# Kernel optimization log

Measured on AMD Instinct MI355X. Metric: run time of the kernel, lower is better.

The kernel has to match this reference:

```python
import jax, jax.numpy as jnp
import numpy as np

B, N, D, HID, S, NH = 2, 384, 768, 256, 64, 8


def layernorm(x, g, b, eps=1e-5):
    m = x.mean(-1, keepdims=True)
    v = ((x - m) ** 2).mean(-1, keepdims=True)
    return (x - m) * jax.lax.rsqrt(v + eps) * g + b


def setup_inputs() -> dict:
    key = jax.random.key(0)
    ks = jax.random.split(key, 32)
    r = lambda i, shp: jax.random.normal(ks[i], shp, dtype=jnp.float32) * 0.02
    inp = {
        'coordinates': jax.random.normal(ks[0], (B, N, 3), dtype=jnp.float32),
        'features': jax.random.normal(ks[1], (B, N, D), dtype=jnp.float32),
        'superpoint_labels': jax.random.randint(ks[2], (B, N), 0, S),
        # geometric_encoder: Linear(9,HID)-LN-ReLU-Linear(HID,D)-LN
        'ge_w1': r(3, (9, HID)), 'ge_b1': jnp.zeros((HID,)),
        'ge_g1': jnp.ones((HID,)), 'ge_be1': jnp.zeros((HID,)),
        'ge_w2': r(4, (HID, D)), 'ge_b2': jnp.zeros((D,)),
        'ge_g2': jnp.ones((D,)), 'ge_be2': jnp.zeros((D,)),
        # superpoint_aggregator: Linear(D,HID)-LN-ReLU-Linear(HID,D)-LN
        'ag_w1': r(5, (D, HID)), 'ag_b1': jnp.zeros((HID,)),
        'ag_g1': jnp.ones((HID,)), 'ag_be1': jnp.zeros((HID,)),
        'ag_w2': r(6, (HID, D)), 'ag_b2': jnp.zeros((D,)),
        'ag_g2': jnp.ones((D,)), 'ag_be2': jnp.zeros((D,)),
        # spatial_attention (MultiheadAttention, 8 heads)
        'wq': r(7, (D, D)), 'bq': jnp.zeros((D,)),
        'wk': r(8, (D, D)), 'bk': jnp.zeros((D,)),
        'wv': r(9, (D, D)), 'bv': jnp.zeros((D,)),
        'wo': r(10, (D, D)), 'bo': jnp.zeros((D,)),
    }
    return inp


def _forward(coordinates, features, superpoint_labels,
             ge_w1, ge_b1, ge_g1, ge_be1, ge_w2, ge_b2, ge_g2, ge_be2,
             ag_w1, ag_b1, ag_g1, ag_be1, ag_w2, ag_b2, ag_g2, ag_be2,
             wq, bq, wk, bk, wv, bv, wo, bo):
    # pairwise geometric relations: [B,N,N,9]
    rp = coordinates[:, :, None, :] - coordinates[:, None, :, :]
    dist = jnp.linalg.norm(rp, axis=-1, keepdims=True)
    rn = rp / jnp.maximum(dist, 1e-12)  # F.normalize semantics
    z = jnp.zeros_like(rn[..., 0])
    # torch loop writes channels (i*3+j-3): (0,1)->-2==3, (0,2)->-1==4, (1,2)->2; ch 0,1 stay zero
    ang = jnp.stack([z, z, rn[..., 1] * rn[..., 2],
                     rn[..., 0] * rn[..., 1], rn[..., 0] * rn[..., 2]], axis=-1)
    rel = jnp.concatenate([dist, rn, ang], axis=-1)
    h = jax.nn.relu(layernorm(rel @ ge_w1 + ge_b1, ge_g1, ge_be1))
    enc = layernorm(h @ ge_w2 + ge_b2, ge_g2, ge_be2)  # [B,N,N,D]
    geo_ctx = enc.mean(axis=2)  # [B,N,D]
    # per-superpoint scatter-mean (vectorized over all groups)
    oh = jax.nn.one_hot(superpoint_labels, S, dtype=features.dtype)  # [B,N,S]
    cnt = oh.sum(axis=1)  # [B,S]
    denom = jnp.maximum(cnt, 1.0)[..., None]
    mean_f = jnp.einsum('bns,bnd->bsd', oh, features) / denom
    mean_g = jnp.einsum('bns,bnd->bsd', oh, geo_ctx) / denom
    ah = jax.nn.relu(layernorm(mean_f @ ag_w1 + ag_b1, ag_g1, ag_be1))
    agg = layernorm(ah @ ag_w2 + ag_b2, ag_g2, ag_be2)
    combined = agg + mean_g  # [B,S,D]
    bidx = jnp.arange(B)[:, None]
    comb_g = combined[bidx, superpoint_labels]  # gather back [B,N,D]
    valid = (cnt[bidx, superpoint_labels] >= 2.0)[..., None]
    cw = 0.3  # consistency_weight
    enhanced = jnp.where(valid, (1.0 - cw) * features + cw * comb_g, features)
    # cross-attention: q=enhanced, k=v=geo_ctx
    dh = D // NH
    q = (enhanced @ wq + bq).reshape(B, N, NH, dh).transpose(0, 2, 1, 3)
    k = (geo_ctx @ wk + bk).reshape(B, N, NH, dh).transpose(0, 2, 1, 3)
    v = (geo_ctx @ wv + bv).reshape(B, N, NH, dh).transpose(0, 2, 1, 3)
    attn = jax.nn.softmax(jnp.einsum('bhqd,bhkd->bhqk', q, k) * (dh ** -0.5), axis=-1)
    o = jnp.einsum('bhqk,bhkd->bhqd', attn, v).transpose(0, 2, 1, 3).reshape(B, N, D)
    spatial = o @ wo + bo
    return enhanced + 0.5 * spatial


def reference(coordinates, features, superpoint_labels,
              ge_w1, ge_b1, ge_g1, ge_be1, ge_w2, ge_b2, ge_g2, ge_be2,
              ag_w1, ag_b1, ag_g1, ag_be1, ag_w2, ag_b2, ag_g2, ag_be2,
              wq, bq, wk, bk, wv, bv, wo, bo):
    return _forward(coordinates, features, superpoint_labels,
                    ge_w1, ge_b1, ge_g1, ge_be1, ge_w2, ge_b2, ge_g2, ge_be2,
                    ag_w1, ag_b1, ag_g1, ag_be1, ag_w2, ag_b2, ag_g2, ag_be2,
                    wq, bq, wk, bk, wv, bv, wo, bo)
```

## Files before the change

### kernel.cpp

```cpp
#include <hip/hip_runtime.h>
#include <hip/hip_bf16.h>
#include <stdint.h>
#include <stddef.h>

#define BB 2
#define NN 384
#define DD 768
#define HH 256
#define SS 64
#define NHH 8
#define DHH 96

typedef __attribute__((ext_vector_type(8))) short bf16x8;
typedef __attribute__((ext_vector_type(4))) float f32x4;

__device__ __forceinline__ float bits_f(unsigned short u){
  unsigned x = ((unsigned)u) << 16; float f; __builtin_memcpy(&f, &x, 4); return f;
}
__device__ __forceinline__ unsigned short f_bits(float a){
  unsigned x; __builtin_memcpy(&x, &a, 4);
  unsigned r = x + 0x7fffu + ((x >> 16) & 1u);
  return (unsigned short)(r >> 16);
}
__device__ __forceinline__ float lo_f(unsigned u){ unsigned x = u << 16; float f; __builtin_memcpy(&f,&x,4); return f; }
__device__ __forceinline__ float hi_f(unsigned u){ unsigned x = u & 0xffff0000u; float f; __builtin_memcpy(&f,&x,4); return f; }
__device__ __forceinline__ unsigned cvt_pk_bf16(float a, float b){
  unsigned r; asm("v_cvt_pk_bf16_f32 %0, %1, %2" : "=v"(r) : "v"(a), "v"(b));
  return r;
}

__global__ __launch_bounds__(256) void k_prep(
    const float* __restrict__ w2, const float* __restrict__ w1g,
    const float* __restrict__ wq, const float* __restrict__ wk,
    const float* __restrict__ wv, const float* __restrict__ wo,
    const float* __restrict__ aw1, const float* __restrict__ aw2,
    short* __restrict__ w2T, short* __restrict__ w2r,
    short* __restrict__ wqT, short* __restrict__ wkT, short* __restrict__ wvT,
    short* __restrict__ woT, short* __restrict__ w1t,
    short* __restrict__ agw1T, short* __restrict__ agw2T)
{
  __shared__ short tile[64*66];
  const int tid = threadIdx.x, blk = blockIdx.x;
  if (blk < 48){
    int t = blk;
    int r0 = (t/12)*64, c0 = (t%12)*64;
    int g = tid >> 6, c = tid & 63;
    #pragma unroll
    for (int i=0;i<16;++i){
      int r = i*4 + g;
      tile[r*66 + c] = (short)f_bits(w2[(size_t)(r0+r)*768 + c0 + c]);
    }
    __syncthreads();
    #pragma unroll
    for (int i=0;i<16;++i){
      int cc = i*4 + g, rr = c;
      w2T[(size_t)(c0+cc)*256 + r0 + rr] = tile[rr*66 + cc];
    }
    return;
  }
  if (blk < 816){
    int idx = (blk-48)*256 + tid;
    w2r[idx] = (short)f_bits(w2[idx]);
    return;
  }
  if (blk < 1392){
    int t = blk - 816;
    int mat = t / 144, tt = t % 144;
    const float* W = (mat==0)?wq:(mat==1)?wk:(mat==2)?wv:wo;
    short* T = (mat==0)?wqT:(mat==1)?wkT:(mat==2)?wvT:woT;
    int r0 = (tt/12)*64, c0 = (tt%12)*64;
    int g = tid >> 6, c = tid & 63;
    #pragma unroll
    for (int i=0;i<16;++i){
      int r = i*4 + g;
      tile[r*66 + c] = (short)f_bits(W[(size_t)(r0+r)*768 + c0 + c]);
    }
    __syncthreads();
    #pragma unroll
    for (int i=0;i<16;++i){
      int cc = i*4 + g, rr = c;
      T[(size_t)(c0+cc)*768 + r0 + rr] = tile[rr*66 + cc];
    }
    return;
  }
  if (blk < 1424){
    int idx = (blk-1392)*256 + tid;
    int c = idx >> 5, kk = idx & 31;
    w1t[idx] = (kk < 9) ? (short)f_bits(w1g[kk*256 + c]) : (short)0;
    return;
  }
  if (blk < 1472){
    int t = blk - 1424;
    int r0 = (t/4)*64, c0 = (t%4)*64;
    int g = tid >> 6, c = tid & 63;
    #pragma unroll
    for (int i=0;i<16;++i){
      int r = i*4 + g;
      tile[r*66 + c] = (short)f_bits(aw1[(size_t)(r0+r)*256 + c0 + c]);
    }
    __syncthreads();
    #pragma unroll
    for (int i=0;i<16;++i){
      int cc = i*4 + g, rr = c;
      agw1T[(size_t)(c0+cc)*768 + r0 + rr] = tile[rr*66 + cc];
    }
    return;
  }
  {
    int t = blk - 1472;
    int r0 = (t/12)*64, c0 = (t%12)*64;
    int g = tid >> 6, c = tid & 63;
    #pragma unroll
    for (int i=0;i<16;++i){
      int r = i*4 + g;
      tile[r*66 + c] = (short)f_bits(aw2[(size_t)(r0+r)*768 + c0 + c]);
    }
    __syncthreads();
    #pragma unroll
    for (int i=0;i<16;++i){
      int cc = i*4 + g, rr = c;
      agw2T[(size_t)(c0+cc)*256 + r0 + rr] = tile[rr*66 + cc];
    }
  }
}

__global__ __launch_bounds__(256) void k_gprep(const short* __restrict__ w2r,
                                               const float* __restrict__ b2,
                                               const short* __restrict__ w1t,
                                               const float* __restrict__ b1,
                                               short* __restrict__ Gm, float* __restrict__ gscal,
                                               float* __restrict__ g1s){
  __shared__ float b2s[768];
  __shared__ float red[8];
  const int tid = threadIdx.x, blk = blockIdx.x;
  if (blk < 64){
    const int wave = tid >> 6, lane = tid & 63, quad = lane >> 4, l16 = lane & 15;
    const int id = blk*4 + wave, ti = id >> 4, tj = id & 15;
    f32x4 acc = (f32x4){0.f,0.f,0.f,0.f};
    for (int ks = 0; ks < 24; ++ks){
      bf16x8 af = *(const bf16x8*)&w2r[(size_t)(ti*16 + l16)*768 + ks*32 + quad*8];
      bf16x8 bf = *(const bf16x8*)&w2r[(size_t)(tj*16 + l16)*768 + ks*32 + quad*8];
      acc = __builtin_amdgcn_mfma_f32_16x16x32_bf16(af, bf, acc, 0,0,0);
    }
    #pragma unroll
    for (int r = 0; r < 4; ++r)
      Gm[(ti*16 + quad*4 + r)*256 + tj*16 + l16] = (short)f_bits(acc[r]);
  } else if (blk == 64){
    for (int c = tid; c < 768; c += 256) b2s[c] = b2[c];
    __syncthreads();
    float sa = 0.f, wa = 0.f;
    const uint4* wr = (const uint4*)(w2r + (size_t)tid*768);
    #pragma unroll 4
    for (int kk = 0; kk < 96; ++kk){
      uint4 ww = wr[kk];
      const float* bp = &b2s[kk*8];
      float x0=lo_f(ww.x), x1=hi_f(ww.x), x2=lo_f(ww.y), x3=hi_f(ww.y);
      float x4=lo_f(ww.z), x5=hi_f(ww.z), x6=lo_f(ww.w), x7=hi_f(ww.w);
      sa += (x0+x1)+(x2+x3)+(x4+x5)+(x6+x7);
      wa += bp[0]*x0 + bp[1]*x1 + bp[2]*x2 + bp[3]*x3
          + bp[4]*x4 + bp[5]*x5 + bp[6]*x6 + bp[7]*x7;
    }
    Gm[256*256 + tid] = (short)f_bits(sa);
    Gm[257*256 + tid] = (short)f_bits(wa);
    #pragma unroll
    for (int rr = 258; rr < 288; ++rr) Gm[rr*256 + tid] = 0;
    float pb = 0.f, pbb = 0.f;
    for (int c = tid; c < 768; c += 256){ float bb = b2s[c]; pb += bb; pbb += bb*bb; }
    for (int m = 32; m >= 1; m >>= 1){ pb += __shfl_xor(pb,m); pbb += __shfl_xor(pbb,m); }
    if ((tid & 63) == 0){ red[tid>>6] = pb; red[4+(tid>>6)] = pbb; }
    __syncthreads();
    if (tid == 0){ gscal[0] = red[0]+red[1]+red[2]+red[3]; gscal[1] = red[4]+red[5]+red[6]+red[7]; }
  } else {
    const unsigned short* w1u = (const unsigned short*)w1t;
    if (tid < 81){
      int i = tid / 9, j = tid % 9;
      float acc = 0.f;
      for (int c = 0; c < 256; ++c)
        acc += bits_f(w1u[c*32 + i]) * bits_f(w1u[c*32 + j]);
      g1s[18 + tid] = acc;
    } else if (tid < 90){
      int i = tid - 81;
      float sa = 0.f, sb = 0.f;
      for (int c = 0; c < 256; ++c){
        float x = bits_f(w1u[c*32 + i]);
        sa += x; sb += x * b1[c];
      }
      g1s[i] = sa; g1s[9 + i] = sb;
    } else if (tid == 90){
      float pb = 0.f, pbb = 0.f;
      for (int c = 0; c < 256; ++c){ float bb = b1[c]; pb += bb; pbb += bb*bb; }
      g1s[99] = pb; g1s[100] = pbb;
    }
  }
}

__global__ __launch_bounds__(256, 3) void k_geo(
    const float* __restrict__ coord, const short* __restrict__ w1t,
    const float* __restrict__ b1g, const float* __restrict__ g1g, const float* __restrict__ be1g,
    const short* __restrict__ Gm, const float* __restrict__ gscal,
    const float* __restrict__ g1s, float* __restrict__ gv)
{
  __shared__ short relbf[64*36];
  __shared__ short h_bf[64*256];
  __shared__ float rmean[64], rrstd[64];
  __shared__ float msum[64], wbsum[64], qsum[64];

  const int tid = threadIdx.x;
  const int pair = blockIdx.x % 768;
  const int jt   = blockIdx.x / 768;
  const int j0 = jt * 64;
  const int b = pair / NN;

  if (tid < 64){
    int j = j0 + tid;
    float cix = coord[pair*3+0], ciy = coord[pair*3+1], ciz = coord[pair*3+2];
    float dx = cix - coord[(b*NN+j)*3+0];
    float dy = ciy - coord[(b*NN+j)*3+1];
    float dz = ciz - coord[(b*NN+j)*3+2];
    float dist = sqrtf(dx*dx + dy*dy + dz*dz);
    float inv = 1.f / fmaxf(dist, 1e-12f);
    float x = dx*inv, y = dy*inv, z = dz*inv;
    float rv[9];
    rv[0]=dist; rv[1]=x; rv[2]=y; rv[3]=z; rv[4]=0.f; rv[5]=0.f;
    rv[6]=y*z; rv[7]=x*y; rv[8]=x*z;
    short* rr = &relbf[tid*36];
    float rbf[9];
    #pragma unroll
    for (int k=0;k<9;++k){
      unsigned short hb = f_bits(rv[k]);
      rr[k] = (short)hb; rbf[k] = bits_f(hb);
    }
    #pragma unroll
    for (int k=9;k<32;++k) rr[k]=0;
    float s = g1s[99], ssq = g1s[100];
    #pragma unroll
    for (int i=0;i<9;++i){
      s += rbf[i]*g1s[i];
      ssq += 2.f*rbf[i]*g1s[9+i];
      #pragma unroll
      for (int jj=0;jj<9;++jj) ssq += rbf[i]*rbf[jj]*g1s[18+i*9+jj];
    }
    float mean = s*(1.f/256.f);
    float var  = ssq*(1.f/256.f) - mean*mean;
    rmean[tid] = mean; rrstd[tid] = rsqrtf(var + 1e-5f);
  } else if (tid < 128){
    qsum[tid-64] = 0.f;
  }
  __syncthreads();

  const int wave = tid >> 6, lane = tid & 63, quad = lane >> 4, l16 = lane & 15;

  unsigned hreg[4][4][2];
  {
    bf16x8 af[4];
    #pragma unroll
    for (int rb=0;rb<4;++rb)
      af[rb] = *(const bf16x8*)&relbf[(rb*16 + l16)*36 + quad*8];
    f32x4 hacc[4][4];
    #pragma unroll
    for (int ci=0;ci<4;++ci){
      int cb = wave*4 + ci;
      bf16x8 bfw = *(const bf16x8*)&w1t[(cb*16 + l16)*32 + quad*8];
      #pragma unroll
      for (int rb=0;rb<4;++rb)
        hacc[ci][rb] = __builtin_amdgcn_mfma_f32_16x16x32_bf16(af[rb], bfw, (f32x4){0.f,0.f,0.f,0.f}, 0,0,0);
    }
    f32x4 rmv[4], rsv[4];
    #pragma unroll
    for (int rb=0;rb<4;++rb){
      rmv[rb] = *(const f32x4*)&rmean[rb*16 + quad*4];
      rsv[rb] = *(const f32x4*)&rrstd[rb*16 + quad*4];
    }
    #pragma unroll
    for (int ci=0;ci<4;++ci){
      int col = (wave*4+ci)*16 + l16;
      float b1c = b1g[col], g1c = g1g[col], be1c = be1g[col];
      int chb = col >> 3, lo = col & 7;
      #pragma unroll
      for (int rb=0;rb<4;++rb){
        float hn[4];
        #pragma unroll
        for (int r=0;r<4;++r)
          hn[r] = fmaxf((hacc[ci][rb][r] + b1c - rmv[rb][r]) * rsv[rb][r] * g1c + be1c, 0.f);
        unsigned p0 = cvt_pk_bf16(hn[0], hn[1]);
        unsigned p1 = cvt_pk_bf16(hn[2], hn[3]);
        hreg[ci][rb][0] = p0; hreg[ci][rb][1] = p1;
        int row0 = rb*16 + quad*4;
        h_bf[(row0+0)*256 + ((chb + row0+0)&31)*8 + lo] = (short)(p0 & 0xffff);
        h_bf[(row0+1)*256 + ((chb + row0+1)&31)*8 + lo] = (short)(p0 >> 16);
        h_bf[(row0+2)*256 + ((chb + row0+2)&31)*8 + lo] = (short)(p1 & 0xffff);
        h_bf[(row0+3)*256 + ((chb + row0+3)&31)*8 + lo] = (short)(p1 >> 16);
      }
    }
  }
  __syncthreads();

  {
    f32x4 acc[4][4];
    #pragma unroll
    for (int ci=0;ci<4;++ci)
      #pragma unroll
      for (int rb=0;rb<4;++rb) acc[ci][rb] = (f32x4){0.f,0.f,0.f,0.f};
    f32x4 eacc[4];
    #pragma unroll
    for (int rb=0;rb<4;++rb) eacc[rb] = (f32x4){0.f,0.f,0.f,0.f};
    for (int ks=0;ks<8;++ks){
      bf16x8 a4[4];
      #pragma unroll
      for (int rb=0;rb<4;++rb){
        int row = rb*16 + l16;
        a4[rb] = *(const bf16x8*)&h_bf[row*256 + (((ks*4 + quad) + row)&31)*8];
      }
      #pragma unroll
      for (int ci=0;ci<4;++ci){
        int n = (wave*4+ci)*16 + l16;
        bf16x8 bg = *(const bf16x8*)&Gm[n*256 + ks*32 + quad*8];
        #pragma unroll
        for (int rb=0;rb<4;++rb)
          acc[ci][rb] = __builtin_amdgcn_mfma_f32_16x16x32_bf16(a4[rb], bg, acc[ci][rb], 0,0,0);
      }
      if (wave == 0){
        bf16x8 bge = *(const bf16x8*)&Gm[(256 + l16)*256 + ks*32 + quad*8];
        #pragma unroll
        for (int rb=0;rb<4;++rb)
          eacc[rb] = __builtin_amdgcn_mfma_f32_16x16x32_bf16(a4[rb], bge, eacc[rb], 0,0,0);
      }
    }
    if (wave == 0 && l16 < 2){
      float* dst = (l16 == 0) ? msum : wbsum;
      #pragma unroll
      for (int rb=0;rb<4;++rb)
        #pragma unroll
        for (int r=0;r<4;++r) dst[rb*16 + quad*4 + r] = eacc[rb][r];
    }
    #pragma unroll
    for (int rb=0;rb<4;++rb){
      #pragma unroll
      for (int r=0;r<4;++r){
        int row = rb*16 + quad*4 + r;
        float qp = 0.f;
        #pragma unroll
        for (int ci=0;ci<4;++ci){
          unsigned p = hreg[ci][rb][r>>1];
          float hv = (r & 1) ? hi_f(p) : lo_f(p);
          qp += acc[ci][rb][r] * hv;
        }
        qp += __shfl_xor(qp,1);
        qp += __shfl_xor(qp,2);
        qp += __shfl_xor(qp,4);
        qp += __shfl_xor(qp,8);
        if (l16 == 0) atomicAdd(&qsum[row], qp);
      }
    }
  }
  __syncthreads();
  if (tid < 64){
    float Sb = gscal[0], Sbb = gscal[1];
    float m2 = (msum[tid] + Sb)*(1.f/768.f);
    float ssq = qsum[tid] + 2.f*wbsum[tid] + Sbb;
    float var = ssq*(1.f/768.f) - m2*m2;
    rmean[tid] = m2; rrstd[tid] = rsqrtf(var + 1e-5f);
  }
  __syncthreads();
  float* gp = gv + ((size_t)pair*6 + jt)*258;
  if (tid < 64){
    float rr = rrstd[tid], tt = rmean[tid]*rrstd[tid];
    for (int m = 32; m >= 1; m >>= 1){ rr += __shfl_xor(rr,m); tt += __shfl_xor(tt,m); }
    if (tid == 0){ gp[256] = rr; gp[257] = tt; }
  }
  {
    float vp[4] = {0.f, 0.f, 0.f, 0.f};
    #pragma unroll
    for (int rb=0;rb<4;++rb){
      #pragma unroll
      for (int r=0;r<4;++r){
        int row = rb*16 + quad*4 + r;
        float rs = rrstd[row];
        #pragma unroll
        for (int ci=0;ci<4;++ci){
          unsigned p = hreg[ci][rb][r>>1];
          float hv = (r & 1) ? hi_f(p) : lo_f(p);
          vp[ci] += rs * hv;
        }
      }
    }
    #pragma unroll
    for (int ci=0;ci<4;++ci){
      vp[ci] += __shfl_xor(vp[ci],16);
      vp[ci] += __shfl_xor(vp[ci],32);
    }
    if (quad == 0){
      #pragma unroll
      for (int ci=0;ci<4;++ci)
        gp[(wave*4+ci)*16 + l16] = vp[ci];
    }
  }
}

__global__ __launch_bounds__(256) void k_geofin(
    const float* __restrict__ gv, const short* __restrict__ w2r,
    const float* __restrict__ b2g, const float* __restrict__ g2g,
    const float* __restrict__ be2g, unsigned short* __restrict__ geo)
{
  __shared__ float V[256];
  __shared__ float RT[2];
  const int tid = threadIdx.x, pair = blockIdx.x;
  const float* gp = gv + (size_t)pair*6*258;
  V[tid] = gp[tid] + gp[258 + tid] + gp[2*258 + tid]
         + gp[3*258 + tid] + gp[4*258 + tid] + gp[5*258 + tid];
  if (tid < 2){
    float r = 0.f;
    #pragma unroll
    for (int t = 0; t < 6; ++t) r += gp[t*258 + 256 + tid];
    RT[tid] = r;
  }
  __syncthreads();
  const float R = RT[0], T = RT[1];
  const unsigned short* wr = (const unsigned short*)w2r;
  float a0 = 0.f, a1 = 0.f, a2 = 0.f;
  #pragma unroll 4
  for (int k = 0; k < 256; ++k){
    float vk = V[k];
    const unsigned short* row = wr + (size_t)k*768;
    a0 += vk * bits_f(row[tid]);
    a1 += vk * bits_f(row[tid+256]);
    a2 += vk * bits_f(row[tid+512]);
  }
  size_t base = (size_t)pair*DD;
  geo[base + tid]       = f_bits(g2g[tid]    *(a0 + b2g[tid]    *R - T)*(1.f/384.f) + be2g[tid]);
  geo[base + tid + 256] = f_bits(g2g[tid+256]*(a1 + b2g[tid+256]*R - T)*(1.f/384.f) + be2g[tid+256]);
  geo[base + tid + 512] = f_bits(g2g[tid+512]*(a2 + b2g[tid+512]*R - T)*(1.f/384.f) + be2g[tid+512]);
}

__global__ __launch_bounds__(256) void k_agg(
    const int* __restrict__ lab, const float* __restrict__ feat,
    const unsigned short* __restrict__ geo, float* __restrict__ cntw,
    const short* __restrict__ w1T, const float* __restrict__ b1g,
    const float* __restrict__ g1g, const float* __restrict__ be1g,
    const short* __restrict__ w2T, const float* __restrict__ b2g,
    const float* __restrict__ g2g, const float* __restrict__ be2g,
    float* __restrict__ comb)
{
  __shared__ int ls[NN];
  __shared__ float xr[DD];
  __shared__ float hr[HH];
  __shared__ float red[8];
  const int tid = threadIdx.x;
  const int bs = blockIdx.x, b = bs >> 6, s = bs & 63;
  for (int j = tid; j < NN; j += 256) ls[j] = lab[b*NN + j];
  __syncthreads();
  float f0 = 0.f, f1 = 0.f, f2 = 0.f, gg0 = 0.f, gg1 = 0.f, gg2 = 0.f;
  int cnt = 0;
  for (int j = 0; j < NN; ++j){
    if (ls[j] == s){
      ++cnt;
      size_t rb = (size_t)(b*NN + j)*DD;
      f0  += feat[rb + tid];
      f1  += feat[rb + tid + 256];
      f2  += feat[rb + tid + 512];
      gg0 += bits_f(geo[rb + tid]);
      gg1 += bits_f(geo[rb + tid + 256]);
      gg2 += bits_f(geo[rb + tid + 512]);
    }
  }
  const float inv = 1.f / fmaxf((float)cnt, 1.f);
  if (tid == 0) cntw[bs] = (float)cnt;
  xr[tid]       = f0*inv;
  xr[tid + 256] = f1*inv;
  xr[tid + 512] = f2*inv;
  float gmean[3] = { gg0*inv, gg1*inv, gg2*inv };
  __syncthreads();
  float a = b1g[tid];
  {
    const uint4* wr = (const uint4*)(w1T + (size_t)tid*768);
    #pragma unroll 4
    for (int kk = 0; kk < 96; ++kk){
      uint4 ww = wr[kk];
      const float* xp = &xr[kk*8];
      a += xp[0]*lo_f(ww.x) + xp[1]*hi_f(ww.x)
         + xp[2]*lo_f(ww.y) + xp[3]*hi_f(ww.y)
         + xp[4]*lo_f(ww.z) + xp[5]*hi_f(ww.z)
         + xp[6]*lo_f(ww.w) + xp[7]*hi_f(ww.w);
    }
  }
  float sum1 = a, q1 = a*a;
  for (int m = 32; m >= 1; m >>= 1){ sum1 += __shfl_xor(sum1,m); q1 += __shfl_xor(q1,m); }
  if ((tid & 63) == 0){ red[tid>>6] = sum1; red[4+(tid>>6)] = q1; }
  __syncthreads();
  sum1 = red[0]+red[1]+red[2]+red[3]; q1 = red[4]+red[5]+red[6]+red[7];
  float mean = sum1*(1.f/HH), var = q1*(1.f/HH) - mean*mean, rstd = rsqrtf(var + 1e-5f);
  float h = fmaxf((a-mean)*rstd*g1g[tid] + be1g[tid], 0.f);
  hr[tid] = h;
  __syncthreads();
  float y[3];
  #pragma unroll
  for (int u = 0; u < 3; ++u){
    int c = tid + 256*u;
    float t = b2g[c];
    const uint4* wr = (const uint4*)(w2T + (size_t)c*256);
    #pragma unroll 4
    for (int kk = 0; kk < 32; ++kk){
      uint4 ww = wr[kk];
      const float* hp = &hr[kk*8];
      t += hp[0]*lo_f(ww.x) + hp[1]*hi_f(ww.x)
         + hp[2]*lo_f(ww.y) + hp[3]*hi_f(ww.y)
         + hp[4]*lo_f(ww.z) + hp[5]*hi_f(ww.z)
         + hp[6]*lo_f(ww.w) + hp[7]*hi_f(ww.w);
    }
    y[u] = t;
  }
  float s2 = y[0]+y[1]+y[2], q2 = y[0]*y[0]+y[1]*y[1]+y[2]*y[2];
  for (int m = 32; m >= 1; m >>= 1){ s2 += __shfl_xor(s2,m); q2 += __shfl_xor(q2,m); }
  __syncthreads();
  if ((tid & 63) == 0){ red[tid>>6] = s2; red[4+(tid>>6)] = q2; }
  __syncthreads();
  s2 = red[0]+red[1]+red[2]+red[3]; q2 = red[4]+red[5]+red[6]+red[7];
  float mean2 = s2*(1.f/DD), rstd2 = rsqrtf(q2*(1.f/DD) - mean2*mean2 + 1e-5f);
  size_t base = (size_t)bs * DD;
  #pragma unroll
  for (int u = 0; u < 3; ++u){
    int c = tid + 256*u;
    comb[base + c] = (y[u]-mean2)*rstd2*g2g[c] + be2g[c] + gmean[u];
  }
}

__global__ void k_enhance(const float* __restrict__ feat, const int* __restrict__ lab,
                          const float* __restrict__ cntw, const float* __restrict__ comb,
                          float* __restrict__ enh, unsigned short* __restrict__ enhb)
{
  int idx = blockIdx.x * 256 + threadIdx.x;
  int c = idx % DD; int bn = idx / DD; int b = bn / NN;
  int l = lab[bn];
  float f = feat[idx];
  float cg = comb[(size_t)(b*SS + l)*DD + c];
  float cnt = cntw[b*SS + l];
  float e = (cnt >= 2.0f) ? (0.7f*f + 0.3f*cg) : f;
  enh[idx] = e;
  enhb[idx] = f_bits(e);
}

__global__ __launch_bounds__(256, 4) void k_qkv(
    const unsigned short* __restrict__ enhb, const unsigned short* __restrict__ geo,
    const short* __restrict__ wqT, const short* __restrict__ wkT, const short* __restrict__ wvT,
    const float* __restrict__ bq, const float* __restrict__ bk, const float* __restrict__ bv,
    unsigned short* __restrict__ qo, unsigned short* __restrict__ ko, unsigned short* __restrict__ vo)
{
  const int tid = threadIdx.x, blk = blockIdx.x;
  const int m = blk / 144, rem = blk % 144;
  const int rt = rem / 3, ct = rem % 3;
  const int wave = tid >> 6, lane = tid & 63, quad = lane >> 4, l16 = lane & 15;
  const short* WT = (m==0)?wqT:(m==1)?wkT:wvT;
  const float* Bv = (m==0)?bq:(m==1)?bk:bv;
  unsigned short* Y = (m==0)?qo:(m==1)?ko:vo;
  const short* X = (const short*)((m==0)? enhb : geo);
  const float oscale = (m==0)? 0.10206207261596577f : 1.0f;
  const int row0 = rt*16;
  const int col0 = ct*256 + wave*64;

  f32x4 acc[4];
  #pragma unroll
  for (int cb=0;cb<4;++cb) acc[cb] = (f32x4){0.f,0.f,0.f,0.f};
  for (int ks = 0; ks < 24; ++ks){
    bf16x8 af = *(const bf16x8*)&X[(size_t)(row0 + l16)*DD + ks*32 + quad*8];
    #pragma unroll
    for (int cb=0;cb<4;++cb){
      bf16x8 bw = *(const bf16x8*)&WT[(size_t)(col0 + cb*16 + l16)*DD + ks*32 + quad*8];
      acc[cb] = __builtin_amdgcn_mfma_f32_16x16x32_bf16(af, bw, acc[cb], 0,0,0);
    }
  }
  #pragma unroll
  for (int cb=0;cb<4;++cb){
    int col = col0 + cb*16 + l16;
    float bb = Bv[col];
    #pragma unroll
    for (int r=0;r<4;++r){
      int row = row0 + quad*4 + r;
      Y[(size_t)row*DD + col] = f_bits((acc[cb][r] + bb)*oscale);
    }
  }
}

__global__ __launch_bounds__(256) void k_attn_split(
    const unsigned short* __restrict__ qws, const unsigned short* __restrict__ kws,
    const unsigned short* __restrict__ vws, float* __restrict__ pws)
{
  __shared__ short kt[64*104];
  __shared__ short vt[64*104];
  __shared__ float st[32*66];
  __shared__ float lsum[32];
  const int tid = threadIdx.x;
  const int half = blockIdx.x / 192;
  const int inner = blockIdx.x % 192;
  const int b = inner / (NHH*12); int rem = inner % (NHH*12);
  const int h = rem / 12; const int qt = rem % 12; const int q0 = qt*32;
  const int sq = tid >> 3, jp = tid & 7;
  const int qp = tid >> 4, dp = tid & 15;
  unsigned qreg[48];
  {
    const unsigned* qr = (const unsigned*)(qws + (size_t)(b*NN + q0 + sq)*DD + h*DHH);
    #pragma unroll
    for (int d2 = 0; d2 < 48; ++d2) qreg[d2] = qr[d2];
  }
  if (tid < 32) lsum[tid] = 0.f;
  float Oacc[2][6];
  #pragma unroll
  for (int a = 0; a < 2; ++a)
    #pragma unroll
    for (int m = 0; m < 6; ++m) Oacc[a][m] = 0.f;

  for (int jt = half*3; jt < half*3 + 3; ++jt){
    const int j0 = jt * 64;
    __syncthreads();
    for (int x = tid; x < 64*48; x += 256){
      int jl = x / 48, du = x % 48;
      size_t rowoff = (size_t)(b*NN + j0 + jl)*DD + h*DHH;
      ((unsigned*)&kt[jl*104])[du] = ((const unsigned*)(kws + rowoff))[du];
      ((unsigned*)&vt[jl*104])[du] = ((const unsigned*)(vws + rowoff))[du];
    }
    __syncthreads();
    float lpart = 0.f;
    #pragma unroll
    for (int jj = 0; jj < 8; ++jj){
      int j = jp*8 + jj;
      const uint4* kr4 = (const uint4*)&kt[j*104];
      float s = 0.f;
      #pragma unroll
      for (int d4 = 0; d4 < 12; ++d4){
        uint4 kk = kr4[d4];
        unsigned q0r = qreg[4*d4], q1r = qreg[4*d4+1], q2r = qreg[4*d4+2], q3r = qreg[4*d4+3];
        s += lo_f(kk.x)*lo_f(q0r) + hi_f(kk.x)*hi_f(q0r);
        s += lo_f(kk.y)*lo_f(q1r) + hi_f(kk.y)*hi_f(q1r);
        s += lo_f(kk.z)*lo_f(q2r) + hi_f(kk.z)*hi_f(q2r);
        s += lo_f(kk.w)*lo_f(q3r) + hi_f(kk.w)*hi_f(q3r);
      }
      float p = __expf(s);
      st[sq*66 + j] = p;
      lpart += p;
    }
    lpart += __shfl_xor(lpart,1);
    lpart += __shfl_xor(lpart,2);
    lpart += __shfl_xor(lpart,4);
    if (jp == 0) lsum[sq] += lpart;
    __syncthreads();
    #pragma unroll 4
    for (int j = 0; j < 64; ++j){
      float p0 = st[(2*qp)*66 + j];
      float p1 = st[(2*qp+1)*66 + j];
      const unsigned* vr = (const unsigned*)&vt[j*104 + dp*6];
      #pragma unroll
      for (int m = 0; m < 3; ++m){
        unsigned vv = vr[m];
        float v0 = lo_f(vv), v1 = hi_f(vv);
        Oacc[0][2*m]   += p0*v0; Oacc[0][2*m+1] += p0*v1;
        Oacc[1][2*m]   += p1*v0; Oacc[1][2*m+1] += p1*v1;
      }
    }
  }
  __syncthreads();
  float* pb = pws + ((size_t)inner*2 + half)*3104;
  #pragma unroll
  for (int m = 0; m < 6; ++m){
    pb[(2*qp)*96 + dp*6 + m]   = Oacc[0][m];
    pb[(2*qp+1)*96 + dp*6 + m] = Oacc[1][m];
  }
  if (tid < 32) pb[3072 + tid] = lsum[tid];
}

__global__ __launch_bounds__(256) void k_attnfin(
    const float* __restrict__ pws, unsigned short* __restrict__ ows)
{
  __shared__ float ls[32];
  const int tid = threadIdx.x, inner = blockIdx.x;
  const int b = inner / (NHH*12); int rem = inner % (NHH*12);
  const int h = rem / 12; const int qt = rem % 12; const int q0 = qt*32;
  const float* p0 = pws + (size_t)inner*2*3104;
  const float* p1 = p0 + 3104;
  if (tid < 32) ls[tid] = 1.f / (p0[3072+tid] + p1[3072+tid]);
  __syncthreads();
  #pragma unroll
  for (int u = 0; u < 12; ++u){
    int e = tid + u*256;
    int q = e / 96, d = e % 96;
    float o = (p0[e] + p1[e]) * ls[q];
    ows[(size_t)(b*NN + q0 + q)*DD + h*DHH + d] = f_bits(o);
  }
}

__global__ __launch_bounds__(256) void k_attn_full(
    const unsigned short* __restrict__ qws, const unsigned short* __restrict__ kws,
    const unsigned short* __restrict__ vws, unsigned short* __restrict__ ows)
{
  __shared__ short kt[64*104];
  __shared__ short vt[64*104];
  __shared__ float st[32*66];
  __shared__ float lsum[32];
  const int tid = threadIdx.x;
  const int blk = blockIdx.x;
  const int b = blk / (NHH*12); int rem = blk % (NHH*12);
  const int h = rem / 12; const int qt = rem % 12; const int q0 = qt*32;
  const int sq = tid >> 3, jp = tid & 7;
  const int qp = tid >> 4, dp = tid & 15;
  unsigned qreg[48];
  {
    const unsigned* qr = (const unsigned*)(qws + (size_t)(b*NN + q0 + sq)*DD + h*DHH);
    #pragma unroll
    for (int d2 = 0; d2 < 48; ++d2) qreg[d2] = qr[d2];
  }
  if (tid < 32) lsum[tid] = 0.f;
  float Oacc[2][6];
  #pragma unroll
  for (int a = 0; a < 2; ++a)
    #pragma unroll
    for (int m = 0; m < 6; ++m) Oacc[a][m] = 0.f;
  for (int jt = 0; jt < 6; ++jt){
    const int j0 = jt * 64;
    __syncthreads();
    for (int x = tid; x < 64*48; x += 256){
      int jl = x / 48, du = x % 48;
      size_t rowoff = (size_t)(b*NN + j0 + jl)*DD + h*DHH;
      ((unsigned*)&kt[jl*104])[du] = ((const unsigned*)(kws + rowoff))[du];
      ((unsigned*)&vt[jl*104])[du] = ((const unsigned*)(vws + rowoff))[du];
    }
    __syncthreads();
    float lpart = 0.f;
    #pragma unroll
    for (int jj = 0; jj < 8; ++jj){
      int j = jp*8 + jj;
      const uint4* kr4 = (const uint4*)&kt[j*104];
      float s = 0.f;
      #pragma unroll
      for (int d4 = 0; d4 < 12; ++d4){
        uint4 kk = kr4[d4];
        unsigned q0r = qreg[4*d4], q1r = qreg[4*d4+1], q2r = qreg[4*d4+2], q3r = qreg[4*d4+3];
        s += lo_f(kk.x)*lo_f(q0r) + hi_f(kk.x)*hi_f(q0r);
        s += lo_f(kk.y)*lo_f(q1r) + hi_f(kk.y)*hi_f(q1r);
        s += lo_f(kk.z)*lo_f(q2r) + hi_f(kk.z)*hi_f(q2r);
        s += lo_f(kk.w)*lo_f(q3r) + hi_f(kk.w)*hi_f(q3r);
      }
      float p = __expf(s);
      st[sq*66 + j] = p;
      lpart += p;
    }
    lpart += __shfl_xor(lpart,1);
    lpart += __shfl_xor(lpart,2);
    lpart += __shfl_xor(lpart,4);
    if (jp == 0) lsum[sq] += lpart;
    __syncthreads();
    #pragma unroll 4
    for (int j = 0; j < 64; ++j){
      float p0 = st[(2*qp)*66 + j];
      float p1 = st[(2*qp+1)*66 + j];
      const unsigned* vr = (const unsigned*)&vt[j*104 + dp*6];
      #pragma unroll
      for (int m = 0; m < 3; ++m){
        unsigned vv = vr[m];
        float v0 = lo_f(vv), v1 = hi_f(vv);
        Oacc[0][2*m]   += p0*v0; Oacc[0][2*m+1] += p0*v1;
        Oacc[1][2*m]   += p1*v0; Oacc[1][2*m+1] += p1*v1;
      }
    }
  }
  __syncthreads();
  float l0 = 1.f / lsum[2*qp], l1 = 1.f / lsum[2*qp+1];
  size_t ob = (size_t)(b*NN + q0)*DD + h*DHH + dp*6;
  #pragma unroll
  for (int m = 0; m < 6; ++m){
    ows[ob + (size_t)(2*qp)*DD + m]   = f_bits(Oacc[0][m]*l0);
    ows[ob + (size_t)(2*qp+1)*DD + m] = f_bits(Oacc[1][m]*l1);
  }
}

__global__ __launch_bounds__(256, 4) void k_out(
    const unsigned short* __restrict__ ows, const float* __restrict__ enh,
    const short* __restrict__ woT, const float* __restrict__ bo, float* __restrict__ out)
{
  const int tid = threadIdx.x, blk = blockIdx.x;
  const int rt = blk / 3, ct = blk % 3;
  const int wave = tid >> 6, lane = tid & 63, quad = lane >> 4, l16 = lane & 15;
  const int row0 = rt*16;
  const int col0 = ct*256 + wave*64;
  f32x4 acc[4];
  #pragma unroll
  for (int cb=0;cb<4;++cb) acc[cb] = (f32x4){0.f,0.f,0.f,0.f};
  for (int ks = 0; ks < 24; ++ks){
    bf16x8 af = *(const bf16x8*)&((const short*)ows)[(size_t)(row0 + l16)*DD + ks*32 + quad*8];
    #pragma unroll
    for (int cb=0;cb<4;++cb){
      bf16x8 bw = *(const bf16x8*)&woT[(size_t)(col0 + cb*16 + l16)*DD + ks*32 + quad*8];
      acc[cb] = __builtin_amdgcn_mfma_f32_16x16x32_bf16(af, bw, acc[cb], 0,0,0);
    }
  }
  #pragma unroll
  for (int cb=0;cb<4;++cb){
    int col = col0 + cb*16 + l16;
    float bb = bo[col];
    #pragma unroll
    for (int r=0;r<4;++r){
      size_t idx = (size_t)(row0 + quad*4 + r)*DD + col;
      out[idx] = enh[idx] + 0.5f*(acc[cb][r] + bb);
    }
  }
}

extern "C" void kernel_launch(void* const* d_in, const int* in_sizes, int n_in,
                              void* d_out, int out_size, void* d_ws, size_t ws_size,
                              hipStream_t stream) {
  const float* coord = (const float*)d_in[0];
  const float* feat  = (const float*)d_in[1];
  const int*   lab   = (const int*)d_in[2];
  const float* ge_w1 = (const float*)d_in[3];
  const float* ge_b1 = (const float*)d_in[4];
  const float* ge_g1 = (const float*)d_in[5];
  const float* ge_be1= (const float*)d_in[6];
  const float* ge_w2 = (const float*)d_in[7];
  const float* ge_b2 = (const float*)d_in[8];
  const float* ge_g2 = (const float*)d_in[9];
  const float* ge_be2= (const float*)d_in[10];
  const float* ag_w1 = (const float*)d_in[11];
  const float* ag_b1 = (const float*)d_in[12];
  const float* ag_g1 = (const float*)d_in[13];
  const float* ag_be1= (const float*)d_in[14];
  const float* ag_w2 = (const float*)d_in[15];
  const float* ag_b2 = (const float*)d_in[16];
  const float* ag_g2 = (const float*)d_in[17];
  const float* ag_be2= (const float*)d_in[18];
  const float* wq = (const float*)d_in[19];
  const float* bq = (const float*)d_in[20];
  const float* wk = (const float*)d_in[21];
  const float* bk = (const float*)d_in[22];
  const float* wv = (const float*)d_in[23];
  const float* bv = (const float*)d_in[24];
  const float* wo = (const float*)d_in[25];
  const float* bo = (const float*)d_in[26];

  char* w = (char*)d_ws;
  unsigned short* geo_bf = (unsigned short*)(w);
  float*          enh_f  = (float*)(w + 1179648);
  unsigned short* enh_bf = (unsigned short*)(w + 3538944);
  unsigned short* qw_bf  = (unsigned short*)(w + 4718592);
  unsigned short* kw_bf  = (unsigned short*)(w + 5898240);
  unsigned short* vw_bf  = (unsigned short*)(w + 7077888);
  float*          gv     = (float*)(w + 4718592);
  float*          cntw   = (float*)(w + 9842688);
  float*          comb   = (float*)(w + 9843200);
  short*          w2T    = (short*)(w + 10236416);
  short*          w2r    = (short*)(w + 10629632);
  short*          w1t    = (short*)(w + 11022848);
  short*          Gm     = (short*)(w + 11039232);
  float*          g1s    = (float*)(w + 11186688);
  float*          gscal  = (float*)(w + 11187200);
  short*          wqT    = (short*)(w + 11187456);
  short*          wkT    = (short*)(w + 12367104);
  short*          wvT    = (short*)(w + 13546752);
  short*          woT    = (short*)(w + 14726400);
  short*          agw1T  = (short*)(w + 15906048);
  short*          agw2T  = (short*)(w + 16299264);
  float*          pws    = (float*)(w + 16692480);
  unsigned short* ow_bf  = geo_bf;
  const bool split_attn = (ws_size >= 21460224);

  hipLaunchKernelGGL(k_prep,    dim3(1520),  dim3(256), 0, stream,
                     ge_w2, ge_w1, wq, wk, wv, wo, ag_w1, ag_w2,
                     w2T, w2r, wqT, wkT, wvT, woT, w1t, agw1T, agw2T);
  hipLaunchKernelGGL(k_gprep,   dim3(66),    dim3(256), 0, stream,
                     w2r, ge_b2, w1t, ge_b1, Gm, gscal, g1s);
  hipLaunchKernelGGL(k_geo,     dim3(4608),  dim3(256), 0, stream,
                     coord, w1t, ge_b1, ge_g1, ge_be1, Gm, gscal, g1s, gv);
  hipLaunchKernelGGL(k_geofin,  dim3(768),   dim3(256), 0, stream,
                     gv, w2r, ge_b2, ge_g2, ge_be2, geo_bf);
  hipLaunchKernelGGL(k_agg,     dim3(128),   dim3(256), 0, stream,
                     lab, feat, geo_bf, cntw, agw1T, ag_b1, ag_g1, ag_be1,
                     agw2T, ag_b2, ag_g2, ag_be2, comb);
  hipLaunchKernelGGL(k_enhance, dim3(2304),  dim3(256), 0, stream,
                     feat, lab, cntw, comb, enh_f, enh_bf);
  hipLaunchKernelGGL(k_qkv,     dim3(432),   dim3(256), 0, stream,
                     enh_bf, geo_bf, wqT, wkT, wvT, bq, bk, bv, qw_bf, kw_bf, vw_bf);
  if (split_attn){
    hipLaunchKernelGGL(k_attn_split, dim3(384), dim3(256), 0, stream,
                       qw_bf, kw_bf, vw_bf, pws);
    hipLaunchKernelGGL(k_attnfin,    dim3(192), dim3(256), 0, stream,
                       pws, ow_bf);
  } else {
    hipLaunchKernelGGL(k_attn_full,  dim3(192), dim3(256), 0, stream,
                       qw_bf, kw_bf, vw_bf, ow_bf);
  }
  hipLaunchKernelGGL(k_out,     dim3(144),   dim3(256), 0, stream,
                     ow_bf, enh_f, woT, bo, (float*)d_out);
}
```

Before: 426.6 us.

## Fuse geometric finalize into k_geo by looping over all j-tiles per block

k_geo now assigns one block per point pair and loops over the six 64-column j-tiles internally, accumulating the per-channel projection sums and LayerNorm statistics in registers. The separate k_geofin kernel is folded in, so the partial-sum buffer no longer makes a round trip through global memory and one launch is removed. The final W2 projection now reads a transposed bf16 weight with 16-byte vector loads instead of strided scalar loads. The trade-off is that the grid shrinks from 4608 blocks to 768, which reduces parallelism and latency hiding, and each block does six serialized tile iterations with extra barriers.

```diff
diff --git a/kernel.cpp b/kernel.cpp
--- a/kernel.cpp
+++ b/kernel.cpp
@@ -198,178 +198,184 @@
     const float* __restrict__ coord, const short* __restrict__ w1t,
     const float* __restrict__ b1g, const float* __restrict__ g1g, const float* __restrict__ be1g,
     const short* __restrict__ Gm, const float* __restrict__ gscal,
-    const float* __restrict__ g1s, float* __restrict__ gv)
+    const float* __restrict__ g1s, const short* __restrict__ w2Tg,
+    const float* __restrict__ b2g, const float* __restrict__ g2g,
+    const float* __restrict__ be2g, unsigned short* __restrict__ geo)
 {
   __shared__ short relbf[64*36];
   __shared__ short h_bf[64*256];
   __shared__ float rmean[64], rrstd[64];
   __shared__ float msum[64], wbsum[64], qsum[64];
+  __shared__ float Vsh[256];
+  __shared__ float RT[2];
 
   const int tid = threadIdx.x;
-  const int pair = blockIdx.x % 768;
-  const int jt   = blockIdx.x / 768;
-  const int j0 = jt * 64;
+  const int pair = blockIdx.x;
   const int b = pair / NN;
-
+  const int wave = tid >> 6, lane = tid & 63, quad = lane >> 4, l16 = lane & 15;
+
+  float cix = 0.f, ciy = 0.f, ciz = 0.f;
   if (tid < 64){
-    int j = j0 + tid;
-    float cix = coord[pair*3+0], ciy = coord[pair*3+1], ciz = coord[pair*3+2];
-    float dx = cix - coord[(b*NN+j)*3+0];
-    float dy = ciy - coord[(b*NN+j)*3+1];
-    float dz = ciz - coord[(b*NN+j)*3+2];
-    float dist = sqrtf(dx*dx + dy*dy + dz*dz);
-    float inv = 1.f / fmaxf(dist, 1e-12f);
-    float x = dx*inv, y = dy*inv, z = dz*inv;
-    float rv[9];
-    rv[0]=dist; rv[1]=x; rv[2]=y; rv[3]=z; rv[4]=0.f; rv[5]=0.f;
-    rv[6]=y*z; rv[7]=x*y; rv[8]=x*z;
-    short* rr = &relbf[tid*36];
-    float rbf[9];
-    #pragma unroll
-    for (int k=0;k<9;++k){
-      unsigned short hb = f_bits(rv[k]);
-      rr[k] = (short)hb; rbf[k] = bits_f(hb);
-    }
-    #pragma unroll
-    for (int k=9;k<32;++k) rr[k]=0;
-    float s = g1s[99], ssq = g1s[100];
-    #pragma unroll
-    for (int i=0;i<9;++i){
-      s += rbf[i]*g1s[i];
-      ssq += 2.f*rbf[i]*g1s[9+i];
-      #pragma unroll
-      for (int jj=0;jj<9;++jj) ssq += rbf[i]*rbf[jj]*g1s[18+i*9+jj];
-    }
-    float mean = s*(1.f/256.f);
-    float var  = ssq*(1.f/256.f) - mean*mean;
-    rmean[tid] = mean; rrstd[tid] = rsqrtf(var + 1e-5f);
-  } else if (tid < 128){
-    qsum[tid-64] = 0.f;
-  }
-  __syncthreads();
-
-  const int wave = tid >> 6, lane = tid & 63, quad = lane >> 4, l16 = lane & 15;
-
-  unsigned hreg[4][4][2];
-  {
-    bf16x8 af[4];
-    #pragma unroll
-    for (int rb=0;rb<4;++rb)
-      af[rb] = *(const bf16x8*)&relbf[(rb*16 + l16)*36 + quad*8];
-    f32x4 hacc[4][4];
-    #pragma unroll
-    for (int ci=0;ci<4;++ci){
-      int cb = wave*4 + ci;
-      bf16x8 bfw = *(const bf16x8*)&w1t[(cb*16 + l16)*32 + quad*8];
+    cix = coord[pair*3+0]; ciy = coord[pair*3+1]; ciz = coord[pair*3+2];
+  }
+  const float Sb = gscal[0], Sbb = gscal[1];
+  float vp[4] = {0.f, 0.f, 0.f, 0.f};
+  float Racc = 0.f, Tacc = 0.f;
+
+  #pragma unroll 1
+  for (int jt = 0; jt < 6; ++jt){
+    const int j0 = jt * 64;
+    if (tid < 64){
+      int j = j0 + tid;
+      float dx = cix - coord[(b*NN+j)*3+0];
+      float dy = ciy - coord[(b*NN+j)*3+1];
+      float dz = ciz - coord[(b*NN+j)*3+2];
+      float dist = sqrtf(dx*dx + dy*dy + dz*dz);
+      float inv = 1.f / fmaxf(dist, 1e-12f);
+      float x = dx*inv, y = dy*inv, z = dz*inv;
+      float rv[9];
+      rv[0]=dist; rv[1]=x; rv[2]=y; rv[3]=z; rv[4]=0.f; rv[5]=0.f;
+      rv[6]=y*z; rv[7]=x*y; rv[8]=x*z;
+      short* rr = &relbf[tid*36];
+      float rbf[9];
+      #pragma unroll
+      for (int k=0;k<9;++k){
+        unsigned short hb = f_bits(rv[k]);
+        rr[k] = (short)hb; rbf[k] = bits_f(hb);
+      }
+      #pragma unroll
+      for (int k=9;k<32;++k) rr[k]=0;
+      float s = g1s[99], ssq = g1s[100];
+      #pragma unroll
+      for (int i=0;i<9;++i){
+        s += rbf[i]*g1s[i];
+        ssq += 2.f*rbf[i]*g1s[9+i];
+        #pragma unroll
+        for (int jj=0;jj<9;++jj) ssq += rbf[i]*rbf[jj]*g1s[18+i*9+jj];
+      }
+      float mean = s*(1.f/256.f);
+      float var  = ssq*(1.f/256.f) - mean*mean;
+      rmean[tid] = mean; rrstd[tid] = rsqrtf(var + 1e-5f);
+    } else if (tid < 128){
+      qsum[tid-64] = 0.f;
+    }
+    __syncthreads();
+
+    unsigned hreg[4][4][2];
+    {
+      bf16x8 af[4];
       #pragma unroll
       for (int rb=0;rb<4;++rb)
-        hacc[ci][rb] = __builtin_amdgcn_mfma_f32_16x16x32_bf16(af[rb], bfw, (f32x4){0.f,0.f,0.f,0.f}, 0,0,0);
-    }
-    f32x4 rmv[4], rsv[4];
-    #pragma unroll
-    for (int rb=0;rb<4;++rb){
-      rmv[rb] = *(const f32x4*)&rmean[rb*16 + quad*4];
-      rsv[rb] = *(const f32x4*)&rrstd[rb*16 + quad*4];
-    }
-    #pragma unroll
-    for (int ci=0;ci<4;++ci){
-      int col = (wave*4+ci)*16 + l16;
-      float b1c = b1g[col], g1c = g1g[col], be1c = be1g[col];
-      int chb = col >> 3, lo = col & 7;
-      #pragma unroll
-      for (int rb=0;rb<4;++rb){
-        float hn[4];
-        #pragma unroll
-        for (int r=0;r<4;++r)
-          hn[r] = fmaxf((hacc[ci][rb][r] + b1c - rmv[rb][r]) * rsv[rb][r] * g1c + be1c, 0.f);
-        unsigned p0 = cvt_pk_bf16(hn[0], hn[1]);
-        unsigned p1 = cvt_pk_bf16(hn[2], hn[3]);
-        hreg[ci][rb][0] = p0; hreg[ci][rb][1] = p1;
-        int row0 = rb*16 + quad*4;
-        h_bf[(row0+0)*256 + ((chb + row0+0)&31)*8 + lo] = (short)(p0 & 0xffff);
-        h_bf[(row0+1)*256 + ((chb + row0+1)&31)*8 + lo] = (short)(p0 >> 16);
-        h_bf[(row0+2)*256 + ((chb + row0+2)&31)*8 + lo] = (short)(p1 & 0xffff);
-        h_bf[(row0+3)*256 + ((chb + row0+3)&31)*8 + lo] = (short)(p1 >> 16);
-      }
-    }
-  }
-  __syncthreads();
-
-  {
-    f32x4 acc[4][4];
-    #pragma unroll
-    for (int ci=0;ci<4;++ci)
-      #pragma unroll
-      for (int rb=0;rb<4;++rb) acc[ci][rb] = (f32x4){0.f,0.f,0.f,0.f};
-    f32x4 eacc[4];
-    #pragma unroll
-    for (int rb=0;rb<4;++rb) eacc[rb] = (f32x4){0.f,0.f,0.f,0.f};
-    for (int ks=0;ks<8;++ks){
-      bf16x8 a4[4];
-      #pragma unroll
-      for (int rb=0;rb<4;++rb){
-        int row = rb*16 + l16;
-        a4[rb] = *(const bf16x8*)&h_bf[row*256 + (((ks*4 + quad) + row)&31)*8];
-      }
+        af[rb] = *(const bf16x8*)&relbf[(rb*16 + l16)*36 + quad*8];
+      f32x4 hacc[4][4];
       #pragma unroll
       for (int ci=0;ci<4;++ci){
-        int n = (wave*4+ci)*16 + l16;
-        bf16x8 bg = *(const bf16x8*)&Gm[n*256 + ks*32 + quad*8];
+        int cb = wave*4 + ci;
+        bf16x8 bfw = *(const bf16x8*)&w1t[(cb*16 + l16)*32 + quad*8];
         #pragma unroll
         for (int rb=0;rb<4;++rb)
-          acc[ci][rb] = __builtin_amdgcn_mfma_f32_16x16x32_bf16(a4[rb], bg, acc[ci][rb], 0,0,0);
-      }
-      if (wave == 0){
-        bf16x8 bge = *(const bf16x8*)&Gm[(256 + l16)*256 + ks*32 + quad*8];
+          hacc[ci][rb] = __builtin_amdgcn_mfma_f32_16x16x32_bf16(af[rb], bfw, (f32x4){0.f,0.f,0.f,0.f}, 0,0,0);
+      }
+      f32x4 rmv[4], rsv[4];
+      #pragma unroll
+      for (int rb=0;rb<4;++rb){
+        rmv[rb] = *(const f32x4*)&rmean[rb*16 + quad*4];
+        rsv[rb] = *(const f32x4*)&rrstd[rb*16 + quad*4];
+      }
+      #pragma unroll
+      for (int ci=0;ci<4;++ci){
+        int col = (wave*4+ci)*16 + l16;
+        float b1c = b1g[col], g1c = g1g[col], be1c = be1g[col];
+        int chb = col >> 3, lo = col & 7;
+        #pragma unroll
+        for (int rb=0;rb<4;++rb){
+          float hn[4];
+          #pragma unroll
+          for (int r=0;r<4;++r)
+            hn[r] = fmaxf((hacc[ci][rb][r] + b1c - rmv[rb][r]) * rsv[rb][r] * g1c + be1c, 0.f);
+          unsigned p0 = cvt_pk_bf16(hn[0], hn[1]);
+          unsigned p1 = cvt_pk_bf16(hn[2], hn[3]);
+          hreg[ci][rb][0] = p0; hreg[ci][rb][1] = p1;
+          int row0 = rb*16 + quad*4;
+          h_bf[(row0+0)*256 + ((chb + row0+0)&31)*8 + lo] = (short)(p0 & 0xffff);
+          h_bf[(row0+1)*256 + ((chb + row0+1)&31)*8 + lo] = (short)(p0 >> 16);
+          h_bf[(row0+2)*256 + ((chb + row0+2)&31)*8 + lo] = (short)(p1 & 0xffff);
+          h_bf[(row0+3)*256 + ((chb + row0+3)&31)*8 + lo] = (short)(p1 >> 16);
+        }
+      }
+    }
+    __syncthreads();
+
+    {
+      f32x4 acc[4][4];
+      #pragma unroll
+      for (int ci=0;ci<4;++ci)
+        #pragma unroll
+        for (int rb=0;rb<4;++rb) acc[ci][rb] = (f32x4){0.f,0.f,0.f,0.f};
+      f32x4 eacc[4];
+      #pragma unroll
+      for (int rb=0;rb<4;++rb) eacc[rb] = (f32x4){0.f,0.f,0.f,0.f};
+      for (int ks=0;ks<8;++ks){
+        bf16x8 a4[4];
+        #pragma unroll
+        for (int rb=0;rb<4;++rb){
+          int row = rb*16 + l16;
+          a4[rb] = *(const bf16x8*)&h_bf[row*256 + (((ks*4 + quad) + row)&31)*8];
+        }
+        #pragma unroll
+        for (int ci=0;ci<4;++ci){
+          int n = (wave*4+ci)*16 + l16;
+          bf16x8 bg = *(const bf16x8*)&Gm[n*256 + ks*32 + quad*8];
+          #pragma unroll
+          for (int rb=0;rb<4;++rb)
+            acc[ci][rb] = __builtin_amdgcn_mfma_f32_16x16x32_bf16(a4[rb], bg, acc[ci][rb], 0,0,0);
+        }
+        if (wave == 0){
+          bf16x8 bge = *(const bf16x8*)&Gm[(256 + l16)*256 + ks*32 + quad*8];
+          #pragma unroll
+          for (int rb=0;rb<4;++rb)
+            eacc[rb] = __builtin_amdgcn_mfma_f32_16x16x32_bf16(a4[rb], bge, eacc[rb], 0,0,0);
+        }
+      }
+      if (wave == 0 && l16 < 2){
+        float* dst = (l16 == 0) ? msum : wbsum;
         #pragma unroll
         for (int rb=0;rb<4;++rb)
-          eacc[rb] = __builtin_amdgcn_mfma_f32_16x16x32_bf16(a4[rb], bge, eacc[rb], 0,0,0);
-      }
-    }
-    if (wave == 0 && l16 < 2){
-      float* dst = (l16 == 0) ? msum : wbsum;
-      #pragma unroll
-      for (int rb=0;rb<4;++rb)
+          #pragma unroll
+          for (int r=0;r<4;++r) dst[rb*16 + quad*4 + r] = eacc[rb][r];
+      }
+      #pragma unroll
+      for (int rb=0;rb<4;++rb){
         #pragma unroll
-        for (int r=0;r<4;++r) dst[rb*16 + quad*4 + r] = eacc[rb][r];
-    }
-    #pragma unroll
-    for (int rb=0;rb<4;++rb){
-      #pragma unroll
-      for (int r=0;r<4;++r){
-        int row = rb*16 + quad*4 + r;
-        float qp = 0.f;
-        #pragma unroll
-        for (int ci=0;ci<4;++ci){
-          unsigned p = hreg[ci][rb][r>>1];
-          float hv = (r & 1) ? hi_f(p) : lo_f(p);
-          qp += acc[ci][rb][r] * hv;
+        for (int r=0;r<4;++r){
+          int row = rb*16 + quad*4 + r;
+          float qp = 0.f;
+          #pragma unroll
+          for (int ci=0;ci<4;++ci){
+            unsigned p = hreg[ci][rb][r>>1];
+            float hv = (r & 1) ? hi_f(p) : lo_f(p);
+            qp += acc[ci][rb][r] * hv;
+          }
+          qp += __shfl_xor(qp,1);
+          qp += __shfl_xor(qp,2);
+          qp += __shfl_xor(qp,4);
+          qp += __shfl_xor(qp,8);
+          if (l16 == 0) atomicAdd(&qsum[row], qp);
         }
-        qp += __shfl_xor(qp,1);
-        qp += __shfl_xor(qp,2);
-        qp += __shfl_xor(qp,4);
-        qp += __shfl_xor(qp,8);
-        if (l16 == 0) atomicAdd(&qsum[row], qp);
-      }
-    }
-  }
-  __syncthreads();
-  if (tid < 64){
-    float Sb = gscal[0], Sbb = gscal[1];
-    float m2 = (msum[tid] + Sb)*(1.f/768.f);
-    float ssq = qsum[tid] + 2.f*wbsum[tid] + Sbb;
-    float var = ssq*(1.f/768.f) - m2*m2;
-    rmean[tid] = m2; rrstd[tid] = rsqrtf(var + 1e-5f);
-  }
-  __syncthreads();
-  float* gp = gv + ((size_t)pair*6 + jt)*258;
-  if (tid < 64){
-    float rr = rrstd[tid], tt = rmean[tid]*rrstd[tid];
-    for (int m = 32; m >= 1; m >>= 1){ rr += __shfl_xor(rr,m); tt += __shfl_xor(tt,m); }
-    if (tid == 0){ gp[256] = rr; gp[257] = tt; }
-  }
-  {
-    float vp[4] = {0.f, 0.f, 0.f, 0.f};
+      }
+    }
+    __syncthreads();
+
+    if (tid < 64){
+      float m2 = (msum[tid] + Sb)*(1.f/768.f);
+      float ssq = qsum[tid] + 2.f*wbsum[tid] + Sbb;
+      float var = ssq*(1.f/768.f) - m2*m2;
+      float rs = rsqrtf(var + 1e-5f);
+      rrstd[tid] = rs;
+      Racc += rs; Tacc += m2*rs;
+    }
+    __syncthreads();
+
     #pragma unroll
     for (int rb=0;rb<4;++rb){
       #pragma unroll
@@ -384,52 +390,49 @@
         }
       }
     }
-    #pragma unroll
-    for (int ci=0;ci<4;++ci){
-      vp[ci] += __shfl_xor(vp[ci],16);
-      vp[ci] += __shfl_xor(vp[ci],32);
-    }
-    if (quad == 0){
-      #pragma unroll
-      for (int ci=0;ci<4;++ci)
-        gp[(wave*4+ci)*16 + l16] = vp[ci];
-    }
-  }
-}
-
-__global__ __launch_bounds__(256) void k_geofin(
-    const float* __restrict__ gv, const short* __restrict__ w2r,
-    const float* __restrict__ b2g, const float* __restrict__ g2g,
-    const float* __restrict__ be2g, unsigned short* __restrict__ geo)
-{
-  __shared__ float V[256];
-  __shared__ float RT[2];
-  const int tid = threadIdx.x, pair = blockIdx.x;
-  const float* gp = gv + (size_t)pair*6*258;
-  V[tid] = gp[tid] + gp[258 + tid] + gp[2*258 + tid]
-         + gp[3*258 + tid] + gp[4*258 + tid] + gp[5*258 + tid];
-  if (tid < 2){
-    float r = 0.f;
-    #pragma unroll
-    for (int t = 0; t < 6; ++t) r += gp[t*258 + 256 + tid];
-    RT[tid] = r;
-  }
-  __syncthreads();
+    __syncthreads();
+  }
+
+  #pragma unroll
+  for (int ci=0;ci<4;++ci){
+    vp[ci] += __shfl_xor(vp[ci],16);
+    vp[ci] += __shfl_xor(vp[ci],32);
+  }
+  if (quad == 0){
+    #pragma unroll
+    for (int ci=0;ci<4;++ci)
+      Vsh[(wave*4+ci)*16 + l16] = vp[ci];
+  }
+  if (tid < 64){
+    for (int m = 32; m >= 1; m >>= 1){ Racc += __shfl_xor(Racc,m); Tacc += __shfl_xor(Tacc,m); }
+    if (tid == 0){ RT[0] = Racc; RT[1] = Tacc; }
+  }
+  __syncthreads();
+
   const float R = RT[0], T = RT[1];
-  const unsigned short* wr = (const unsigned short*)w2r;
-  float a0 = 0.f, a1 = 0.f, a2 = 0.f;
-  #pragma unroll 4
-  for (int k = 0; k < 256; ++k){
-    float vk = V[k];
-    const unsigned short* row = wr + (size_t)k*768;
-    a0 += vk * bits_f(row[tid]);
-    a1 += vk * bits_f(row[tid+256]);
-    a2 += vk * bits_f(row[tid+512]);
+  float a3[3];
+  #pragma unroll
+  for (int u = 0; u < 3; ++u){
+    int c = tid + 256*u;
+    const uint4* wr = (const uint4*)(w2Tg + (size_t)c*256);
+    float t = 0.f;
+    #pragma unroll 4
+    for (int kk = 0; kk < 32; ++kk){
+      uint4 ww = wr[kk];
+      const float* vv = &Vsh[kk*8];
+      t += vv[0]*lo_f(ww.x) + vv[1]*hi_f(ww.x)
+         + vv[2]*lo_f(ww.y) + vv[3]*hi_f(ww.y)
+         + vv[4]*lo_f(ww.z) + vv[5]*hi_f(ww.z)
+         + vv[6]*lo_f(ww.w) + vv[7]*hi_f(ww.w);
+    }
+    a3[u] = t;
   }
   size_t base = (size_t)pair*DD;
-  geo[base + tid]       = f_bits(g2g[tid]    *(a0 + b2g[tid]    *R - T)*(1.f/384.f) + be2g[tid]);
-  geo[base + tid + 256] = f_bits(g2g[tid+256]*(a1 + b2g[tid+256]*R - T)*(1.f/384.f) + be2g[tid+256]);
-  geo[base + tid + 512] = f_bits(g2g[tid+512]*(a2 + b2g[tid+512]*R - T)*(1.f/384.f) + be2g[tid+512]);
+  #pragma unroll
+  for (int u = 0; u < 3; ++u){
+    int c = tid + 256*u;
+    geo[base + c] = f_bits(g2g[c]*(a3[u] + b2g[c]*R - T)*(1.f/384.f) + be2g[c]);
+  }
 }
 
 __global__ __launch_bounds__(256) void k_agg(
@@ -840,7 +843,6 @@
   unsigned short* qw_bf  = (unsigned short*)(w + 4718592);
   unsigned short* kw_bf  = (unsigned short*)(w + 5898240);
   unsigned short* vw_bf  = (unsigned short*)(w + 7077888);
-  float*          gv     = (float*)(w + 4718592);
   float*          cntw   = (float*)(w + 9842688);
   float*          comb   = (float*)(w + 9843200);
   short*          w2T    = (short*)(w + 10236416);
@@ -864,10 +866,9 @@
                      w2T, w2r, wqT, wkT, wvT, woT, w1t, agw1T, agw2T);
   hipLaunchKernelGGL(k_gprep,   dim3(66),    dim3(256), 0, stream,
                      w2r, ge_b2, w1t, ge_b1, Gm, gscal, g1s);
-  hipLaunchKernelGGL(k_geo,     dim3(4608),  dim3(256), 0, stream,
-                     coord, w1t, ge_b1, ge_g1, ge_be1, Gm, gscal, g1s, gv);
-  hipLaunchKernelGGL(k_geofin,  dim3(768),   dim3(256), 0, stream,
-                     gv, w2r, ge_b2, ge_g2, ge_be2, geo_bf);
+  hipLaunchKernelGGL(k_geo,     dim3(768),   dim3(256), 0, stream,
+                     coord, w1t, ge_b1, ge_g1, ge_be1, Gm, gscal, g1s,
+                     w2T, ge_b2, ge_g2, ge_be2, geo_bf);
   hipLaunchKernelGGL(k_agg,     dim3(128),   dim3(256), 0, stream,
                      lab, feat, geo_bf, cntw, agw1T, ag_b1, ag_g1, ag_be1,
                      agw2T, ag_b2, ag_g2, ag_be2, comb);
```

After: 609.4 us. 1.43x slower.
